# Kernel optimization log

Hardware: AMD Instinct MI355X
Metric: run time of the kernel (lower is better)

The kernel has to match this reference:

```python
import jax, jax.numpy as jnp
import numpy as np

NY, NU, NH = 64, 64, 256  # Nhidden=256 -> 128 complex eigen pairs
T, NB = 4096, 32          # horizon, batch


def setup_inputs() -> dict:
    key = jax.random.key(0)
    ks = jax.random.split(key, 9)
    return {
        "y0": jax.random.normal(ks[0], (NB, NY), jnp.float32),
        "U": jax.random.normal(ks[1], (T, NB, NU), jnp.float32),
        "lmbd_cont_real": jax.random.uniform(ks[2], (NH // 2,), jnp.float32),
        "lmbd_cont_imag": jax.random.uniform(ks[3], (NH // 2,), jnp.float32),
        "B": jax.random.normal(ks[4], (NH, NU), jnp.float32) / np.sqrt(NU),
        "W_y2x": jax.random.normal(ks[5], (NH, NY), jnp.float32) / np.sqrt(NY),
        "b_y2x": jax.random.normal(ks[6], (NH,), jnp.float32) * 0.01,
        "W_x2y": jax.random.normal(ks[7], (NY, NH), jnp.float32) / np.sqrt(NH),
        "b_x2y": jax.random.normal(ks[8], (NY,), jnp.float32) * 0.01,
    }


def reference(y0, U, lmbd_cont_real, lmbd_cont_imag, B, W_y2x, b_y2x, W_x2y, b_x2y):
    # where A is the real 2x2-block form of complex eigenvalues
    # lambda = r * exp(i*theta), r = exp(-|re|), theta = (pi/2)*im.
    # Original builds A^n explicitly (O(T^2)); an O(T) scan computes the same math.
    H = B.shape[0] // 2
    Bu = jnp.einsum('tbu,hu->tbh', U, B)          # (T, NB, NH)
    r = jnp.exp(-jnp.abs(lmbd_cont_real))
    theta = (jnp.pi / 2) * lmbd_cont_imag
    lr = r * jnp.cos(theta)                        # Re(lambda), (H,)
    li = r * jnp.sin(theta)                        # Im(lambda), (H,)
    x0 = y0 @ W_y2x.T + b_y2x                      # (NB, NH)
    zr0, zi0 = x0[:, :H], x0[:, H:]
    a, b = Bu[:, :, :H], Bu[:, :, H:]

    def step(carry, inp):
        zr, zi = carry
        ak, bk = inp
        nzr = lr * zr - li * zi + ak
        nzi = li * zr + lr * zi + bk
        return (nzr, nzi), (nzr, nzi)

    _, (Xr, Xi) = jax.lax.scan(step, (zr0, zi0), (a, b))
    X = jnp.concatenate([Xr, Xi], axis=-1)         # (T, NB, NH)
    Y = X @ W_x2y.T + b_x2y                        # (T, NB, NY)
    return Y
```

## Files before the change

kernel.cpp:

```cpp
#include <hip/hip_runtime.h>
#include <math.h>

#define TT   4096
#define NBB  32
#define NUU  64
#define NHH  256
#define HH   128
#define NYY  64
#define LCH  8
#define CCH  512
#define SEGN 16
#define CPS  32

#define PI_HALF 1.5707963267948966f

typedef float  f32x16 __attribute__((ext_vector_type(16)));
typedef __bf16 bf16x8 __attribute__((ext_vector_type(8)));
typedef __bf16 bf16x2 __attribute__((ext_vector_type(2)));
typedef unsigned int uint4v __attribute__((ext_vector_type(4)));

__device__ inline int crow(int r, int lane) { return (r & 3) + 8 * (r >> 2) + 4 * (lane >> 5); }
__device__ inline bf16x8 ldfrag(const unsigned short* p) {
    return __builtin_bit_cast(bf16x8, *(const uint4v*)p);
}

#define CVT(v, H, L) { __bf16 _h = (__bf16)(v); H = _h; L = (__bf16)((v) - (float)_h); }

__device__ inline void lam_f32(float xre, float xim, float& lr, float& li) {
    float th = PI_HALF * xim;
    float rf = (float)exp(-(double)fabsf(xre));
    float cf = (float)cos((double)th);
    float sf = (float)sin((double)th);
    lr = rf * cf; li = rf * sf;
}

__device__ inline int swzU(int row, int so) {
    return row * 128 + ((((so >> 3) ^ row) & 15) << 3) + (so & 7);
}
__device__ inline int swzX(int row, int so) {
    int chv = so >> 3;
    chv = (chv & 32) | ((chv ^ row) & 31);
    return row * 512 + (chv << 3) + (so & 7);
}

__global__ __launch_bounds__(256) void k_prep(
    const float* __restrict__ B, const float* __restrict__ W,
    const float* __restrict__ y0, const float* __restrict__ Wy2x,
    const float* __restrict__ by2x,
    unsigned short* __restrict__ Bph, unsigned short* __restrict__ Bpl,
    unsigned short* __restrict__ Wph, unsigned short* __restrict__ Wpl,
    float2* __restrict__ x0p)
{
    int bx = blockIdx.x, tid = threadIdx.x;
    if (bx < 32) {
        if (tid < HH) {
            int b = bx, ch = tid;
            float xr = by2x[ch], xi = by2x[ch + HH];
            for (int y = 0; y < NYY; ++y) {
                float v = y0[b * NYY + y];
                xr += v * Wy2x[ch * NYY + y];
                xi += v * Wy2x[(ch + HH) * NYY + y];
            }
            x0p[b * HH + ch] = make_float2(xr, xi);
        }
    } else {
        int i = (bx - 32) * 256 + tid;
        float bv = B[i];
        __bf16 bh = (__bf16)bv;
        Bph[i] = __builtin_bit_cast(unsigned short, bh);
        Bpl[i] = __builtin_bit_cast(unsigned short, (__bf16)(bv - (float)bh));
        int y = i >> 8, kidx = i & 255;
        float wv = W[y * NHH + (kidx & 1) * HH + (kidx >> 1)];
        __bf16 wh = (__bf16)wv;
        Wph[i] = __builtin_bit_cast(unsigned short, wh);
        Wpl[i] = __builtin_bit_cast(unsigned short, (__bf16)(wv - (float)wh));
    }
}

__global__ __launch_bounds__(256, 1) void k_pass1(
    const float* __restrict__ U,
    const unsigned short* __restrict__ Bph, const unsigned short* __restrict__ Bpl,
    const float* __restrict__ lre, const float* __restrict__ lim,
    float2* __restrict__ E)
{
    __shared__ __align__(16) unsigned short sU[2][64 * 136];

    const int tid = threadIdx.x, w = tid >> 6, lane = tid & 63;
    const int l31 = lane & 31, kh = lane >> 5;
    const int c = blockIdx.x;
    const int ch = w * 32 + l31;

    float lr, li; lam_f32(lre[ch], lim[ch], lr, li);

    bf16x8 bfh[2][4], bfl[2][4];
#pragma unroll
    for (int nt = 0; nt < 2; ++nt)
#pragma unroll
        for (int kk = 0; kk < 4; ++kk) {
            bfh[nt][kk] = ldfrag(&Bph[(size_t)(nt * HH + ch) * NUU + kk * 16 + kh * 8]);
            bfl[nt][kk] = ldfrag(&Bpl[(size_t)(nt * HH + ch) * NUU + kk * 16 + kh * 8]);
        }

    float zr[16], zi[16];
#pragma unroll
    for (int r = 0; r < 16; ++r) { zr[r] = 0.f; zi[r] = 0.f; }

    const int srow = tid >> 2, sus = (tid & 3) * 16;
    const int sb = srow & 31, stoff = srow >> 5;
    const float* ubase = U + (size_t)sb * NUU + sus;

    float4 f0, f1, f2, f3;
    {
        const float4* sp = (const float4*)(ubase + (size_t)(c * LCH + stoff) * (NBB * NUU));
        f0 = sp[0]; f1 = sp[1]; f2 = sp[2]; f3 = sp[3];
    }

    for (int sub = 0; sub < 4; ++sub) {
        unsigned short* su = &sU[sub & 1][0];
        {
            bf16x8 h0, h1, l0, l1;
            CVT(f0.x, h0[0], l0[0]); CVT(f0.y, h0[1], l0[1]); CVT(f0.z, h0[2], l0[2]); CVT(f0.w, h0[3], l0[3]);
            CVT(f1.x, h0[4], l0[4]); CVT(f1.y, h0[5], l0[5]); CVT(f1.z, h0[6], l0[6]); CVT(f1.w, h0[7], l0[7]);
            CVT(f2.x, h1[0], l1[0]); CVT(f2.y, h1[1], l1[1]); CVT(f2.z, h1[2], l1[2]); CVT(f2.w, h1[3], l1[3]);
            CVT(f3.x, h1[4], l1[4]); CVT(f3.y, h1[5], l1[5]); CVT(f3.z, h1[6], l1[6]); CVT(f3.w, h1[7], l1[7]);
            *(bf16x8*)&su[srow * 136 + sus]          = h0;
            *(bf16x8*)&su[srow * 136 + sus + 8]      = h1;
            *(bf16x8*)&su[srow * 136 + 64 + sus]     = l0;
            *(bf16x8*)&su[srow * 136 + 64 + sus + 8] = l1;
        }
        __syncthreads();

        if (sub < 3) {
            const float4* sp = (const float4*)(ubase + (size_t)(c * LCH + (sub + 1) * 2 + stoff) * (NBB * NUU));
            f0 = sp[0]; f1 = sp[1]; f2 = sp[2]; f3 = sp[3];
        }

        f32x16 acc[2][2];
#pragma unroll
        for (int mt = 0; mt < 2; ++mt)
#pragma unroll
            for (int nt = 0; nt < 2; ++nt)
#pragma unroll
                for (int r = 0; r < 16; ++r) acc[mt][nt][r] = 0.f;

#pragma unroll
        for (int kk = 0; kk < 4; ++kk) {
            bf16x8 a0h = ldfrag(&su[(l31)      * 136 + kk * 16 + kh * 8]);
            bf16x8 a1h = ldfrag(&su[(32 + l31) * 136 + kk * 16 + kh * 8]);
            bf16x8 a0l = ldfrag(&su[(l31)      * 136 + 64 + kk * 16 + kh * 8]);
            bf16x8 a1l = ldfrag(&su[(32 + l31) * 136 + 64 + kk * 16 + kh * 8]);
            acc[0][0] = __builtin_amdgcn_mfma_f32_32x32x16_bf16(a0h, bfh[0][kk], acc[0][0], 0, 0, 0);
            acc[0][1] = __builtin_amdgcn_mfma_f32_32x32x16_bf16(a0h, bfh[1][kk], acc[0][1], 0, 0, 0);
            acc[1][0] = __builtin_amdgcn_mfma_f32_32x32x16_bf16(a1h, bfh[0][kk], acc[1][0], 0, 0, 0);
            acc[1][1] = __builtin_amdgcn_mfma_f32_32x32x16_bf16(a1h, bfh[1][kk], acc[1][1], 0, 0, 0);
            acc[0][0] = __builtin_amdgcn_mfma_f32_32x32x16_bf16(a0l, bfh[0][kk], acc[0][0], 0, 0, 0);
            acc[0][1] = __builtin_amdgcn_mfma_f32_32x32x16_bf16(a0l, bfh[1][kk], acc[0][1], 0, 0, 0);
            acc[1][0] = __builtin_amdgcn_mfma_f32_32x32x16_bf16(a1l, bfh[0][kk], acc[1][0], 0, 0, 0);
            acc[1][1] = __builtin_amdgcn_mfma_f32_32x32x16_bf16(a1l, bfh[1][kk], acc[1][1], 0, 0, 0);
            acc[0][0] = __builtin_amdgcn_mfma_f32_32x32x16_bf16(a0h, bfl[0][kk], acc[0][0], 0, 0, 0);
            acc[0][1] = __builtin_amdgcn_mfma_f32_32x32x16_bf16(a0h, bfl[1][kk], acc[0][1], 0, 0, 0);
            acc[1][0] = __builtin_amdgcn_mfma_f32_32x32x16_bf16(a1h, bfl[0][kk], acc[1][0], 0, 0, 0);
            acc[1][1] = __builtin_amdgcn_mfma_f32_32x32x16_bf16(a1h, bfl[1][kk], acc[1][1], 0, 0, 0);
        }

#pragma unroll
        for (int mt = 0; mt < 2; ++mt)
#pragma unroll
            for (int r = 0; r < 16; ++r) {
                float t0 = fmaf(lr, zr[r], acc[mt][0][r]); t0 = fmaf(-li, zi[r], t0);
                float t1 = fmaf(li, zr[r], acc[mt][1][r]); t1 = fmaf(lr, zi[r], t1);
                zr[r] = t0; zi[r] = t1;
            }
    }

#pragma unroll
    for (int r = 0; r < 16; ++r)
        E[(size_t)c * 4096 + crow(r, lane) * HH + ch] = make_float2(zr[r], zi[r]);
}

__global__ __launch_bounds__(256) void k_cseg(
    const float* __restrict__ lre, const float* __restrict__ lim,
    const float2* __restrict__ E, float2* __restrict__ Esup)
{
    int g = blockIdx.x * 256 + threadIdx.x;
    int chain = g & 4095, seg = g >> 12, ch = chain & 127;
    float lrf, lif; lam_f32(lre[ch], lim[ch], lrf, lif);
    double pr = (double)lrf, pi = (double)lif;
#pragma unroll
    for (int s = 0; s < 3; ++s) { double nr = pr*pr - pi*pi, ni = 2.0*pr*pi; pr = nr; pi = ni; }
    float2 e[CPS];
#pragma unroll
    for (int j = 0; j < CPS; ++j)
        e[j] = E[((size_t)seg * CPS + j) * 4096 + chain];
    double sr = 0.0, si = 0.0;
#pragma unroll
    for (int j = 0; j < CPS; ++j) {
        double nr = pr * sr - pi * si + (double)e[j].x;
        double ni = pi * sr + pr * si + (double)e[j].y;
        sr = nr; si = ni;
    }
    Esup[(size_t)seg * 4096 + chain] = make_float2((float)sr, (float)si);
}

__global__ __launch_bounds__(256) void k_cexp2(
    const float* __restrict__ lre, const float* __restrict__ lim,
    const float2* __restrict__ x0p, const float2* __restrict__ Esup,
    const float2* __restrict__ E, float2* __restrict__ Carry)
{
    int g = blockIdx.x * 256 + threadIdx.x;
    int chain = g & 4095, seg = g >> 12, ch = chain & 127;
    float lrf, lif; lam_f32(lre[ch], lim[ch], lrf, lif);
    double p8r = (double)lrf, p8i = (double)lif;
#pragma unroll
    for (int s = 0; s < 3; ++s) { double nr = p8r*p8r - p8i*p8i, ni = 2.0*p8r*p8i; p8r = nr; p8i = ni; }
    double pr = p8r, pi = p8i;
#pragma unroll
    for (int s = 0; s < 5; ++s) { double nr = pr*pr - pi*pi, ni = 2.0*pr*pi; pr = nr; pi = ni; }
    float2 es[SEGN - 1];
#pragma unroll
    for (int s = 0; s < SEGN - 1; ++s)
        es[s] = Esup[(size_t)s * 4096 + chain];
    float2 c0 = x0p[chain];
    double cr = (double)c0.x, ci = (double)c0.y;
#pragma unroll
    for (int s = 0; s < SEGN - 1; ++s) {
        if (s < seg) {
            double nr = pr * cr - pi * ci + (double)es[s].x;
            double ni = pi * cr + pr * ci + (double)es[s].y;
            cr = nr; ci = ni;
        }
    }
    float2 e[CPS];
#pragma unroll
    for (int j = 0; j < CPS; ++j)
        e[j] = E[((size_t)seg * CPS + j) * 4096 + chain];
#pragma unroll
    for (int j = 0; j < CPS; ++j) {
        Carry[((size_t)seg * CPS + j) * 4096 + chain] = make_float2((float)cr, (float)ci);
        double nr = p8r * cr - p8i * ci + (double)e[j].x;
        double ni = p8i * cr + p8r * ci + (double)e[j].y;
        cr = nr; ci = ni;
    }
}

__global__ __launch_bounds__(256, 1) void k_pass2(
    const float* __restrict__ U,
    const unsigned short* __restrict__ Bph, const unsigned short* __restrict__ Bpl,
    const unsigned short* __restrict__ Wph, const unsigned short* __restrict__ Wpl,
    const float* __restrict__ lre, const float* __restrict__ lim,
    const float* __restrict__ bx2y,
    const float2* __restrict__ Carry, float* __restrict__ Y)
{
    __shared__ __align__(16) unsigned short sU[64 * 128];
    __shared__ __align__(16) unsigned short sX[64 * 512];

    const int tid = threadIdx.x, w = tid >> 6, lane = tid & 63;
    const int l31 = lane & 31, kh = lane >> 5;
    const int c = blockIdx.x;
    const int ch = w * 32 + l31;
    const int mtile = w & 1, ntile = w >> 1;

    float lr, li; lam_f32(lre[ch], lim[ch], lr, li);
    float ybias = bx2y[ntile * 32 + l31];

    bf16x8 bfh[2][4], bfl[2][4];
#pragma unroll
    for (int nt = 0; nt < 2; ++nt)
#pragma unroll
        for (int kk = 0; kk < 4; ++kk) {
            bfh[nt][kk] = ldfrag(&Bph[(size_t)(nt * HH + ch) * NUU + kk * 16 + kh * 8]);
            bfl[nt][kk] = ldfrag(&Bpl[(size_t)(nt * HH + ch) * NUU + kk * 16 + kh * 8]);
        }

    bf16x8 wfh[16], wfl[16];
#pragma unroll
    for (int kk = 0; kk < 16; ++kk) {
        wfh[kk] = ldfrag(&Wph[(size_t)(ntile * 32 + l31) * NHH + kk * 16 + kh * 8]);
        wfl[kk] = ldfrag(&Wpl[(size_t)(ntile * 32 + l31) * NHH + kk * 16 + kh * 8]);
    }

    float zr[16], zi[16];
#pragma unroll
    for (int r = 0; r < 16; ++r) {
        float2 v = Carry[(size_t)c * 4096 + crow(r, lane) * HH + ch];
        zr[r] = v.x; zi[r] = v.y;
    }

    const int srow = tid >> 2, sus = (tid & 3) * 16;
    const int sb = srow & 31, stoff = srow >> 5;
    const float* ubase = U + (size_t)sb * NUU + sus;

    float4 f0, f1, f2, f3;
    {
        const float4* sp = (const float4*)(ubase + (size_t)(c * LCH + stoff) * (NBB * NUU));
        f0 = sp[0]; f1 = sp[1]; f2 = sp[2]; f3 = sp[3];
    }

    for (int sub = 0; sub < 4; ++sub) {
        {
            bf16x8 h0, h1, l0, l1;
            CVT(f0.x, h0[0], l0[0]); CVT(f0.y, h0[1], l0[1]); CVT(f0.z, h0[2], l0[2]); CVT(f0.w, h0[3], l0[3]);
            CVT(f1.x, h0[4], l0[4]); CVT(f1.y, h0[5], l0[5]); CVT(f1.z, h0[6], l0[6]); CVT(f1.w, h0[7], l0[7]);
            CVT(f2.x, h1[0], l1[0]); CVT(f2.y, h1[1], l1[1]); CVT(f2.z, h1[2], l1[2]); CVT(f2.w, h1[3], l1[3]);
            CVT(f3.x, h1[4], l1[4]); CVT(f3.y, h1[5], l1[5]); CVT(f3.z, h1[6], l1[6]); CVT(f3.w, h1[7], l1[7]);
            *(bf16x8*)&sU[swzU(srow, sus)]          = h0;
            *(bf16x8*)&sU[swzU(srow, sus + 8)]      = h1;
            *(bf16x8*)&sU[swzU(srow, 64 + sus)]     = l0;
            *(bf16x8*)&sU[swzU(srow, 64 + sus + 8)] = l1;
        }

        if (sub > 0) {
            f32x16 ya0, ya1, ya2;
#pragma unroll
            for (int r = 0; r < 16; ++r) { ya0[r] = 0.f; ya1[r] = 0.f; ya2[r] = 0.f; }
#pragma unroll
            for (int kk = 0; kk < 16; ++kk) {
                bf16x8 xah = ldfrag(&sX[swzX(mtile * 32 + l31, kk * 16 + kh * 8)]);
                bf16x8 xal = ldfrag(&sX[swzX(mtile * 32 + l31, 256 + kk * 16 + kh * 8)]);
                ya0 = __builtin_amdgcn_mfma_f32_32x32x16_bf16(xah, wfh[kk], ya0, 0, 0, 0);
                ya1 = __builtin_amdgcn_mfma_f32_32x32x16_bf16(xal, wfh[kk], ya1, 0, 0, 0);
                ya2 = __builtin_amdgcn_mfma_f32_32x32x16_bf16(xah, wfl[kk], ya2, 0, 0, 0);
            }
            int t = c * LCH + (sub - 1) * 2 + mtile;
#pragma unroll
            for (int r = 0; r < 16; ++r)
                Y[((size_t)t * NBB + crow(r, lane)) * NYY + ntile * 32 + l31] =
                    (ya0[r] + ya1[r]) + ya2[r] + ybias;
        }
        __syncthreads();

        if (sub < 3) {
            const float4* sp = (const float4*)(ubase + (size_t)(c * LCH + (sub + 1) * 2 + stoff) * (NBB * NUU));
            f0 = sp[0]; f1 = sp[1]; f2 = sp[2]; f3 = sp[3];
        }

        f32x16 acc[2][2];
#pragma unroll
        for (int mt = 0; mt < 2; ++mt)
#pragma unroll
            for (int nt = 0; nt < 2; ++nt)
#pragma unroll
                for (int r = 0; r < 16; ++r) acc[mt][nt][r] = 0.f;

#pragma unroll
        for (int kk = 0; kk < 4; ++kk) {
            bf16x8 a0h = ldfrag(&sU[swzU(l31,      kk * 16 + kh * 8)]);
            bf16x8 a1h = ldfrag(&sU[swzU(32 + l31, kk * 16 + kh * 8)]);
            bf16x8 a0l = ldfrag(&sU[swzU(l31,      64 + kk * 16 + kh * 8)]);
            bf16x8 a1l = ldfrag(&sU[swzU(32 + l31, 64 + kk * 16 + kh * 8)]);
            acc[0][0] = __builtin_amdgcn_mfma_f32_32x32x16_bf16(a0h, bfh[0][kk], acc[0][0], 0, 0, 0);
            acc[0][1] = __builtin_amdgcn_mfma_f32_32x32x16_bf16(a0h, bfh[1][kk], acc[0][1], 0, 0, 0);
            acc[1][0] = __builtin_amdgcn_mfma_f32_32x32x16_bf16(a1h, bfh[0][kk], acc[1][0], 0, 0, 0);
            acc[1][1] = __builtin_amdgcn_mfma_f32_32x32x16_bf16(a1h, bfh[1][kk], acc[1][1], 0, 0, 0);
            acc[0][0] = __builtin_amdgcn_mfma_f32_32x32x16_bf16(a0l, bfh[0][kk], acc[0][0], 0, 0, 0);
            acc[0][1] = __builtin_amdgcn_mfma_f32_32x32x16_bf16(a0l, bfh[1][kk], acc[0][1], 0, 0, 0);
            acc[1][0] = __builtin_amdgcn_mfma_f32_32x32x16_bf16(a1l, bfh[0][kk], acc[1][0], 0, 0, 0);
            acc[1][1] = __builtin_amdgcn_mfma_f32_32x32x16_bf16(a1l, bfh[1][kk], acc[1][1], 0, 0, 0);
            acc[0][0] = __builtin_amdgcn_mfma_f32_32x32x16_bf16(a0h, bfl[0][kk], acc[0][0], 0, 0, 0);
            acc[0][1] = __builtin_amdgcn_mfma_f32_32x32x16_bf16(a0h, bfl[1][kk], acc[0][1], 0, 0, 0);
            acc[1][0] = __builtin_amdgcn_mfma_f32_32x32x16_bf16(a1h, bfl[0][kk], acc[1][0], 0, 0, 0);
            acc[1][1] = __builtin_amdgcn_mfma_f32_32x32x16_bf16(a1h, bfl[1][kk], acc[1][1], 0, 0, 0);
        }

#pragma unroll
        for (int mt = 0; mt < 2; ++mt)
#pragma unroll
            for (int r = 0; r < 16; ++r) {
                float t0 = fmaf(lr, zr[r], acc[mt][0][r]); t0 = fmaf(-li, zi[r], t0);
                float t1 = fmaf(li, zr[r], acc[mt][1][r]); t1 = fmaf(lr, zi[r], t1);
                zr[r] = t0; zi[r] = t1;
                bf16x2 hv, lv;
                { __bf16 _h = (__bf16)t0; hv[0] = _h; lv[0] = (__bf16)(t0 - (float)_h); }
                { __bf16 _h = (__bf16)t1; hv[1] = _h; lv[1] = (__bf16)(t1 - (float)_h); }
                int row = mt * 32 + crow(r, lane);
                *(bf16x2*)&sX[swzX(row, w * 64 + 2 * l31)]       = hv;
                *(bf16x2*)&sX[swzX(row, 256 + w * 64 + 2 * l31)] = lv;
            }
        __syncthreads();
    }

    {
        f32x16 ya0, ya1, ya2;
#pragma unroll
        for (int r = 0; r < 16; ++r) { ya0[r] = 0.f; ya1[r] = 0.f; ya2[r] = 0.f; }
#pragma unroll
        for (int kk = 0; kk < 16; ++kk) {
            bf16x8 xah = ldfrag(&sX[swzX(mtile * 32 + l31, kk * 16 + kh * 8)]);
            bf16x8 xal = ldfrag(&sX[swzX(mtile * 32 + l31, 256 + kk * 16 + kh * 8)]);
            ya0 = __builtin_amdgcn_mfma_f32_32x32x16_bf16(xah, wfh[kk], ya0, 0, 0, 0);
            ya1 = __builtin_amdgcn_mfma_f32_32x32x16_bf16(xal, wfh[kk], ya1, 0, 0, 0);
            ya2 = __builtin_amdgcn_mfma_f32_32x32x16_bf16(xah, wfl[kk], ya2, 0, 0, 0);
        }
        int t = c * LCH + 3 * 2 + mtile;
#pragma unroll
        for (int r = 0; r < 16; ++r)
            Y[((size_t)t * NBB + crow(r, lane)) * NYY + ntile * 32 + l31] =
                (ya0[r] + ya1[r]) + ya2[r] + ybias;
    }
}

extern "C" void kernel_launch(void* const* d_in, const int* in_sizes, int n_in,
                              void* d_out, int out_size, void* d_ws, size_t ws_size,
                              hipStream_t stream) {
    const float* y0    = (const float*)d_in[0];
    const float* U     = (const float*)d_in[1];
    const float* lre   = (const float*)d_in[2];
    const float* lim   = (const float*)d_in[3];
    const float* B     = (const float*)d_in[4];
    const float* W_y2x = (const float*)d_in[5];
    const float* b_y2x = (const float*)d_in[6];
    const float* W_x2y = (const float*)d_in[7];
    const float* b_x2y = (const float*)d_in[8];
    float* Y = (float*)d_out;

    char* p = (char*)d_ws;
    float2* E        = (float2*)p; p += (size_t)CCH * 4096 * sizeof(float2);
    float2* Carry    = (float2*)p; p += (size_t)CCH * 4096 * sizeof(float2);
    float2* Esup     = (float2*)p; p += (size_t)SEGN * 4096 * sizeof(float2);
    float2* x0p      = (float2*)p; p += (size_t)4096 * sizeof(float2);
    unsigned short* Bph = (unsigned short*)p; p += 16384 * sizeof(unsigned short);
    unsigned short* Bpl = (unsigned short*)p; p += 16384 * sizeof(unsigned short);
    unsigned short* Wph = (unsigned short*)p; p += 16384 * sizeof(unsigned short);
    unsigned short* Wpl = (unsigned short*)p; p += 16384 * sizeof(unsigned short);

    k_prep <<<dim3(96),  dim3(256), 0, stream>>>(B, W_x2y, y0, W_y2x, b_y2x, Bph, Bpl, Wph, Wpl, x0p);
    k_pass1<<<dim3(CCH), dim3(256), 0, stream>>>(U, Bph, Bpl, lre, lim, E);
    k_cseg <<<dim3(256), dim3(256), 0, stream>>>(lre, lim, E, Esup);
    k_cexp2<<<dim3(256), dim3(256), 0, stream>>>(lre, lim, x0p, Esup, E, Carry);
    k_pass2<<<dim3(CCH), dim3(256), 0, stream>>>(U, Bph, Bpl, Wph, Wpl, lre, lim, b_x2y, Carry, Y);
}
```

Measured before the change: 170.8 us.

## Fold chunk-local recurrence into lambda-power-weighted B for single GEMM in pass1

Result: no change. 171.5 us (+0.4%).

```diff
diff --git a/kernel.cpp b/kernel.cpp
--- a/kernel.cpp
+++ b/kernel.cpp
@@ -47,8 +47,10 @@
     const float* __restrict__ B, const float* __restrict__ W,
     const float* __restrict__ y0, const float* __restrict__ Wy2x,
     const float* __restrict__ by2x,
+    const float* __restrict__ lre, const float* __restrict__ lim,
     unsigned short* __restrict__ Bph, unsigned short* __restrict__ Bpl,
     unsigned short* __restrict__ Wph, unsigned short* __restrict__ Wpl,
+    unsigned short* __restrict__ Bq2h, unsigned short* __restrict__ Bq2l,
     float2* __restrict__ x0p)
 {
     int bx = blockIdx.x, tid = threadIdx.x;
@@ -63,7 +65,7 @@
             }
             x0p[b * HH + ch] = make_float2(xr, xi);
         }
-    } else {
+    } else if (bx < 96) {
         int i = (bx - 32) * 256 + tid;
         float bv = B[i];
         __bf16 bh = (__bf16)bv;
@@ -74,108 +76,97 @@
         __bf16 wh = (__bf16)wv;
         Wph[i] = __builtin_bit_cast(unsigned short, wh);
         Wpl[i] = __builtin_bit_cast(unsigned short, (__bf16)(wv - (float)wh));
+    } else {
+        int F = (bx - 96) * 256 + tid;
+        int lane = F & 63, kk = (F >> 6) & 31, w = (F >> 11) & 3, nt = (F >> 13) & 1;
+        int l31 = lane & 31, kh = lane >> 5;
+        int ch = w * 32 + l31;
+        int kb = kk * 16 + kh * 8;
+        int j = kb >> 6;
+        float lrf, lif; lam_f32(lre[ch], lim[ch], lrf, lif);
+        double pr = 1.0, pi_ = 0.0;
+        for (int s = 0; s < 7 - j; ++s) {
+            double nr = pr * (double)lrf - pi_ * (double)lif;
+            double ni = pr * (double)lif + pi_ * (double)lrf;
+            pr = nr; pi_ = ni;
+        }
+        for (int e = 0; e < 8; ++e) {
+            int u = (kb + e) & 63;
+            double b0 = (double)B[ch * NUU + u];
+            double b1 = (double)B[(ch + HH) * NUU + u];
+            float val = (nt == 0) ? (float)(pr * b0 - pi_ * b1)
+                                  : (float)(pi_ * b0 + pr * b1);
+            __bf16 vh = (__bf16)val;
+            Bq2h[(size_t)F * 8 + e] = __builtin_bit_cast(unsigned short, vh);
+            Bq2l[(size_t)F * 8 + e] = __builtin_bit_cast(unsigned short, (__bf16)(val - (float)vh));
+        }
     }
 }
 
 __global__ __launch_bounds__(256, 1) void k_pass1(
     const float* __restrict__ U,
-    const unsigned short* __restrict__ Bph, const unsigned short* __restrict__ Bpl,
-    const float* __restrict__ lre, const float* __restrict__ lim,
+    const unsigned short* __restrict__ Bq2h, const unsigned short* __restrict__ Bq2l,
     float2* __restrict__ E)
 {
-    __shared__ __align__(16) unsigned short sU[2][64 * 136];
+    __shared__ __align__(16) unsigned short sL[32 * 1024];
 
     const int tid = threadIdx.x, w = tid >> 6, lane = tid & 63;
     const int l31 = lane & 31, kh = lane >> 5;
     const int c = blockIdx.x;
     const int ch = w * 32 + l31;
 
-    float lr, li; lam_f32(lre[ch], lim[ch], lr, li);
-
-    bf16x8 bfh[2][4], bfl[2][4];
-#pragma unroll
-    for (int nt = 0; nt < 2; ++nt)
-#pragma unroll
-        for (int kk = 0; kk < 4; ++kk) {
-            bfh[nt][kk] = ldfrag(&Bph[(size_t)(nt * HH + ch) * NUU + kk * 16 + kh * 8]);
-            bfl[nt][kk] = ldfrag(&Bpl[(size_t)(nt * HH + ch) * NUU + kk * 16 + kh * 8]);
-        }
-
-    float zr[16], zi[16];
-#pragma unroll
-    for (int r = 0; r < 16; ++r) { zr[r] = 0.f; zi[r] = 0.f; }
-
-    const int srow = tid >> 2, sus = (tid & 3) * 16;
-    const int sb = srow & 31, stoff = srow >> 5;
-    const float* ubase = U + (size_t)sb * NUU + sus;
-
-    float4 f0, f1, f2, f3;
-    {
-        const float4* sp = (const float4*)(ubase + (size_t)(c * LCH + stoff) * (NBB * NUU));
-        f0 = sp[0]; f1 = sp[1]; f2 = sp[2]; f3 = sp[3];
-    }
-
-    for (int sub = 0; sub < 4; ++sub) {
-        unsigned short* su = &sU[sub & 1][0];
-        {
-            bf16x8 h0, h1, l0, l1;
-            CVT(f0.x, h0[0], l0[0]); CVT(f0.y, h0[1], l0[1]); CVT(f0.z, h0[2], l0[2]); CVT(f0.w, h0[3], l0[3]);
-            CVT(f1.x, h0[4], l0[4]); CVT(f1.y, h0[5], l0[5]); CVT(f1.z, h0[6], l0[6]); CVT(f1.w, h0[7], l0[7]);
-            CVT(f2.x, h1[0], l1[0]); CVT(f2.y, h1[1], l1[1]); CVT(f2.z, h1[2], l1[2]); CVT(f2.w, h1[3], l1[3]);
-            CVT(f3.x, h1[4], l1[4]); CVT(f3.y, h1[5], l1[5]); CVT(f3.z, h1[6], l1[6]); CVT(f3.w, h1[7], l1[7]);
-            *(bf16x8*)&su[srow * 136 + sus]          = h0;
-            *(bf16x8*)&su[srow * 136 + sus + 8]      = h1;
-            *(bf16x8*)&su[srow * 136 + 64 + sus]     = l0;
-            *(bf16x8*)&su[srow * 136 + 64 + sus + 8] = l1;
-        }
-        __syncthreads();
-
-        if (sub < 3) {
-            const float4* sp = (const float4*)(ubase + (size_t)(c * LCH + (sub + 1) * 2 + stoff) * (NBB * NUU));
-            f0 = sp[0]; f1 = sp[1]; f2 = sp[2]; f3 = sp[3];
-        }
-
-        f32x16 acc[2][2];
-#pragma unroll
-        for (int mt = 0; mt < 2; ++mt)
-#pragma unroll
-            for (int nt = 0; nt < 2; ++nt)
-#pragma unroll
-                for (int r = 0; r < 16; ++r) acc[mt][nt][r] = 0.f;
-
-#pragma unroll
-        for (int kk = 0; kk < 4; ++kk) {
-            bf16x8 a0h = ldfrag(&su[(l31)      * 136 + kk * 16 + kh * 8]);
-            bf16x8 a1h = ldfrag(&su[(32 + l31) * 136 + kk * 16 + kh * 8]);
-            bf16x8 a0l = ldfrag(&su[(l31)      * 136 + 64 + kk * 16 + kh * 8]);
-            bf16x8 a1l = ldfrag(&su[(32 + l31) * 136 + 64 + kk * 16 + kh * 8]);
-            acc[0][0] = __builtin_amdgcn_mfma_f32_32x32x16_bf16(a0h, bfh[0][kk], acc[0][0], 0, 0, 0);
-            acc[0][1] = __builtin_amdgcn_mfma_f32_32x32x16_bf16(a0h, bfh[1][kk], acc[0][1], 0, 0, 0);
-            acc[1][0] = __builtin_amdgcn_mfma_f32_32x32x16_bf16(a1h, bfh[0][kk], acc[1][0], 0, 0, 0);
-            acc[1][1] = __builtin_amdgcn_mfma_f32_32x32x16_bf16(a1h, bfh[1][kk], acc[1][1], 0, 0, 0);
-            acc[0][0] = __builtin_amdgcn_mfma_f32_32x32x16_bf16(a0l, bfh[0][kk], acc[0][0], 0, 0, 0);
-            acc[0][1] = __builtin_amdgcn_mfma_f32_32x32x16_bf16(a0l, bfh[1][kk], acc[0][1], 0, 0, 0);
-            acc[1][0] = __builtin_amdgcn_mfma_f32_32x32x16_bf16(a1l, bfh[0][kk], acc[1][0], 0, 0, 0);
-            acc[1][1] = __builtin_amdgcn_mfma_f32_32x32x16_bf16(a1l, bfh[1][kk], acc[1][1], 0, 0, 0);
-            acc[0][0] = __builtin_amdgcn_mfma_f32_32x32x16_bf16(a0h, bfl[0][kk], acc[0][0], 0, 0, 0);
-            acc[0][1] = __builtin_amdgcn_mfma_f32_32x32x16_bf16(a0h, bfl[1][kk], acc[0][1], 0, 0, 0);
-            acc[1][0] = __builtin_amdgcn_mfma_f32_32x32x16_bf16(a1h, bfl[0][kk], acc[1][0], 0, 0, 0);
-            acc[1][1] = __builtin_amdgcn_mfma_f32_32x32x16_bf16(a1h, bfl[1][kk], acc[1][1], 0, 0, 0);
-        }
-
-#pragma unroll
-        for (int mt = 0; mt < 2; ++mt)
-#pragma unroll
-            for (int r = 0; r < 16; ++r) {
-                float t0 = fmaf(lr, zr[r], acc[mt][0][r]); t0 = fmaf(-li, zi[r], t0);
-                float t1 = fmaf(li, zr[r], acc[mt][1][r]); t1 = fmaf(lr, zi[r], t1);
-                zr[r] = t0; zi[r] = t1;
-            }
+#pragma unroll
+    for (int p = 0; p < 4; ++p) {
+        int flat0 = p * 4096 + tid * 16;
+        const float4* sp = (const float4*)(U + (size_t)c * 16384 + flat0);
+        float4 f0 = sp[0], f1 = sp[1], f2 = sp[2], f3 = sp[3];
+        int j = flat0 >> 11, b = (flat0 >> 6) & 31, u0 = flat0 & 63;
+        bf16x8 h0, h1, l0, l1;
+        CVT(f0.x, h0[0], l0[0]); CVT(f0.y, h0[1], l0[1]); CVT(f0.z, h0[2], l0[2]); CVT(f0.w, h0[3], l0[3]);
+        CVT(f1.x, h0[4], l0[4]); CVT(f1.y, h0[5], l0[5]); CVT(f1.z, h0[6], l0[6]); CVT(f1.w, h0[7], l0[7]);
+        CVT(f2.x, h1[0], l1[0]); CVT(f2.y, h1[1], l1[1]); CVT(f2.z, h1[2], l1[2]); CVT(f2.w, h1[3], l1[3]);
+        CVT(f3.x, h1[4], l1[4]); CVT(f3.y, h1[5], l1[5]); CVT(f3.z, h1[6], l1[6]); CVT(f3.w, h1[7], l1[7]);
+        int m  = b & 15;
+        int cA = ((j * 8 + (u0 >> 3))     ^ m);
+        int cB = ((j * 8 + (u0 >> 3) + 1) ^ m);
+        *(bf16x8*)&sL[b * 1024 + cA * 8]       = h0;
+        *(bf16x8*)&sL[b * 1024 + cB * 8]       = h1;
+        *(bf16x8*)&sL[b * 1024 + 512 + cA * 8] = l0;
+        *(bf16x8*)&sL[b * 1024 + 512 + cB * 8] = l1;
+    }
+    __syncthreads();
+
+    const unsigned short* b0h = Bq2h + ((size_t)(0 + w) * 32) * 512 + lane * 8;
+    const unsigned short* b1h = Bq2h + ((size_t)(4 + w) * 32) * 512 + lane * 8;
+    const unsigned short* b0l = Bq2l + ((size_t)(0 + w) * 32) * 512 + lane * 8;
+    const unsigned short* b1l = Bq2l + ((size_t)(4 + w) * 32) * 512 + lane * 8;
+
+    f32x16 acc0, acc1;
+#pragma unroll
+    for (int r = 0; r < 16; ++r) { acc0[r] = 0.f; acc1[r] = 0.f; }
+
+    const int m = l31 & 15;
+    const int rowb = l31 * 1024;
+#pragma unroll 4
+    for (int kk = 0; kk < 32; ++kk) {
+        int chs = ((kk * 2 + kh) ^ m) * 8;
+        bf16x8 ah  = ldfrag(&sL[rowb + chs]);
+        bf16x8 al  = ldfrag(&sL[rowb + 512 + chs]);
+        bf16x8 bh0 = ldfrag(b0h + (size_t)kk * 512);
+        bf16x8 bh1 = ldfrag(b1h + (size_t)kk * 512);
+        bf16x8 bl0 = ldfrag(b0l + (size_t)kk * 512);
+        bf16x8 bl1 = ldfrag(b1l + (size_t)kk * 512);
+        acc0 = __builtin_amdgcn_mfma_f32_32x32x16_bf16(ah, bh0, acc0, 0, 0, 0);
+        acc1 = __builtin_amdgcn_mfma_f32_32x32x16_bf16(ah, bh1, acc1, 0, 0, 0);
+        acc0 = __builtin_amdgcn_mfma_f32_32x32x16_bf16(al, bh0, acc0, 0, 0, 0);
+        acc1 = __builtin_amdgcn_mfma_f32_32x32x16_bf16(al, bh1, acc1, 0, 0, 0);
+        acc0 = __builtin_amdgcn_mfma_f32_32x32x16_bf16(ah, bl0, acc0, 0, 0, 0);
+        acc1 = __builtin_amdgcn_mfma_f32_32x32x16_bf16(ah, bl1, acc1, 0, 0, 0);
     }
 
 #pragma unroll
     for (int r = 0; r < 16; ++r)
-        E[(size_t)c * 4096 + crow(r, lane) * HH + ch] = make_float2(zr[r], zi[r]);
+        E[(size_t)c * 4096 + crow(r, lane) * HH + ch] = make_float2(acc0[r], acc1[r]);
 }
 
 __global__ __launch_bounds__(256) void k_cseg(
@@ -418,13 +409,18 @@
     float2* Carry    = (float2*)p; p += (size_t)CCH * 4096 * sizeof(float2);
     float2* Esup     = (float2*)p; p += (size_t)SEGN * 4096 * sizeof(float2);
     float2* x0p      = (float2*)p; p += (size_t)4096 * sizeof(float2);
-    unsigned short* Bph = (unsigned short*)p; p += 16384 * sizeof(unsigned short);
-    unsigned short* Bpl = (unsigned short*)p; p += 16384 * sizeof(unsigned short);
-    unsigned short* Wph = (unsigned short*)p; p += 16384 * sizeof(unsigned short);
-    unsigned short* Wpl = (unsigned short*)p; p += 16384 * sizeof(unsigned short);
-
-    k_prep <<<dim3(96),  dim3(256), 0, stream>>>(B, W_x2y, y0, W_y2x, b_y2x, Bph, Bpl, Wph, Wpl, x0p);
-    k_pass1<<<dim3(CCH), dim3(256), 0, stream>>>(U, Bph, Bpl, lre, lim, E);
+    unsigned short* Bph  = (unsigned short*)p; p += 16384 * sizeof(unsigned short);
+    unsigned short* Bpl  = (unsigned short*)p; p += 16384 * sizeof(unsigned short);
+    unsigned short* Wph  = (unsigned short*)p; p += 16384 * sizeof(unsigned short);
+    unsigned short* Wpl  = (unsigned short*)p; p += 16384 * sizeof(unsigned short);
+    unsigned short* Bq2h = (unsigned short*)p; p += 131072 * sizeof(unsigned short);
+    unsigned short* Bq2l = (unsigned short*)p; p += 131072 * sizeof(unsigned short);
+
+    k_prep <<<dim3(160), dim3(256), 0, stream>>>(B, W_x2y, y0, W_y2x, b_y2x,
+                                                 lre, lim,
+                                                 Bph, Bpl, Wph, Wpl,
+                                                 Bq2h, Bq2l, x0p);
+    k_pass1<<<dim3(CCH), dim3(256), 0, stream>>>(U, Bq2h, Bq2l, E);
     k_cseg <<<dim3(256), dim3(256), 0, stream>>>(lre, lim, E, Esup);
     k_cexp2<<<dim3(256), dim3(256), 0, stream>>>(lre, lim, x0p, Esup, E, Carry);
     k_pass2<<<dim3(CCH), dim3(256), 0, stream>>>(U, Bph, Bpl, Wph, Wpl, lre, lim, b_x2y, Carry, Y);
```
